# Optimization experiments

Measured on AMD Instinct MI355X. Metric: run time of the kernel, lower is better.

The kernel has to match this reference:

```python
import jax, jax.numpy as jnp
import numpy as np

TEMPERATURE = 1.0
CHUNK = 128  # node-block size for the curvature pass


def setup_inputs() -> dict:
    key = jax.random.key(0)
    k1, k2 = jax.random.split(key)
    N, D = 4096, 64
    x = jax.random.normal(k1, (N, D), dtype=jnp.float32)
    # sparse binary adjacency (avg degree ~16) + ring so min degree >= 2
    A = (jax.random.uniform(k2, (N, N)) < 0.004).astype(jnp.float32)
    i = jnp.arange(N)
    A = A.at[i, i].set(0.0)
    A = A.at[i, (i + 1) % N].set(1.0)
    A = A.at[(i + 1) % N, i].set(1.0)
    return {"node_embeddings": x, "adj_matrix": A}


def _physics_components(x, A):
    N, d = x.shape
    mask = A > 0
    deg = jnp.sum(A, axis=-1)                      # [N]

    # ---- total energy ----
    kinetic = jnp.sum(x * x, axis=-1)
    nb = A @ x                                     # neighbor aggregate [N,d]
    potential = -jnp.sum(x * nb, axis=-1)
    total_energy = kinetic + potential / (deg + 1e-8)

    # ---- local entropy over neighbor similarities ----
    xn = x / jnp.maximum(jnp.linalg.norm(x, axis=-1, keepdims=True), 1e-12)
    S = xn @ xn.T                                  # cosine sims [N,N]
    logits = jnp.where(mask, S / TEMPERATURE, -1e30)
    P = jax.nn.softmax(logits, axis=-1)            # masked softmax per row
    local_entropy = -jnp.sum(jnp.where(mask, P * jnp.log(P + 1e-8), 0.0), axis=-1)

    # ---- equilibrium deviation (5-NN local mean in embedding space) ----
    sq = jnp.sum(x * x, axis=-1)
    D2 = jnp.maximum(sq[:, None] + sq[None, :] - 2.0 * (x @ x.T), 1e-12)
    dist = jnp.sqrt(D2)                            # [N,N]
    _, idx = jax.lax.top_k(-dist, 6)               # smallest 6 (self first)
    local_means = jnp.mean(x[idx[:, 1:]], axis=1)  # [N,d]
    gdev = jnp.linalg.norm(x - jnp.mean(x, axis=0, keepdims=True), axis=-1)
    ldev = jnp.linalg.norm(x - local_means, axis=-1)
    equilibrium_deviation = 0.6 * gdev + 0.4 * ldev

    # ---- structural centrality ----
    en = jnp.linalg.norm(x, axis=-1)
    structural_centrality = 0.5 * deg / (N - 1) + 0.5 * en / jnp.max(en)

    # ---- information flow: unbiased var of neighbor sims ----
    ms = jnp.sum(jnp.where(mask, S, 0.0), axis=-1) / deg
    information_flow = jnp.sum(jnp.where(mask, (S - ms[:, None]) ** 2, 0.0), axis=-1) / (deg - 1.0)

    # ---- stability: 1/(1 + mean unbiased var of neighbor embeddings) ----
    m1 = nb / deg[:, None]
    ex2 = A @ (x * x)
    var_dim = (ex2 - deg[:, None] * m1 * m1) / (deg - 1.0)[:, None]
    stability = 1.0 / (1.0 + jnp.mean(var_dim, axis=-1))

    # ---- discrete curvature: 1 - mean pairwise cos angle of centered neighbors ----
    # mean_{j<k} u_j.u_k = (||sum u||^2 - sum ||u||^2) / (deg*(deg-1))
    def body(_, ids):
        xb = x[ids]                                 # [B,d]
        mb = mask[ids]                              # [B,N]
        c = x[None, :, :] - xb[:, None, :]          # [B,N,d]
        nrm = jnp.sqrt(jnp.maximum(jnp.sum(c * c, -1), 1e-12))
        u = jnp.where(mb[..., None], c / jnp.maximum(nrm, 1e-8)[..., None], 0.0)
        s = jnp.sum(u, axis=1)                      # [B,d]
        ssq = jnp.sum(u * u, axis=(1, 2))           # [B]
        db = jnp.sum(mb.astype(x.dtype), axis=-1)
        mean_cos = (jnp.sum(s * s, -1) - ssq) / (db * (db - 1.0))
        return None, 1.0 - mean_cos

    _, curv = jax.lax.scan(body, None, jnp.arange(N).reshape(-1, CHUNK))
    graph_curvature = curv.reshape(N)

    return (total_energy, local_entropy, equilibrium_deviation,
            structural_centrality, information_flow, stability, graph_curvature)


def reference(node_embeddings, adj_matrix):
    return _physics_components(node_embeddings, adj_matrix)
```

## Files before the change

### kernel.cpp

```cpp
#include <hip/hip_runtime.h>
#include <math.h>

#define NN 4096
#define DD 64
#define NSPLIT 16
#define JW 256

typedef _Float16 half8 __attribute__((ext_vector_type(8)));
typedef float f32x4 __attribute__((ext_vector_type(4)));

__device__ __forceinline__ unsigned sxu(unsigned v, int o){
  return (unsigned)__shfl_xor((int)v, o, 64);
}
__device__ __forceinline__ unsigned umn(unsigned a, unsigned b){ return a<b?a:b; }
__device__ __forceinline__ unsigned umx(unsigned a, unsigned b){ return a<b?b:a; }

__device__ __forceinline__ unsigned packkey32(float m, int j){
  float q = fmaf(m, 2048.f, 524288.f);
  q = fminf(fmaxf(q, 0.f), 1048575.f);
  return (((unsigned)q) << 12) | (unsigned)j;
}

__device__ __forceinline__ void ins5u(unsigned k, unsigned b[5]){
  bool c0=k<b[0], c1=k<b[1], c2=k<b[2], c3=k<b[3], c4=k<b[4];
  b[4] = c3 ? b[3] : (c4 ? k : b[4]);
  b[3] = c2 ? b[2] : (c3 ? k : b[3]);
  b[2] = c1 ? b[1] : (c2 ? k : b[2]);
  b[1] = c0 ? b[0] : (c1 ? k : b[1]);
  b[0] = c0 ? k : b[0];
}

__device__ __forceinline__ void mergeStage32(unsigned b[5], int st){
  unsigned p0=sxu(b[0],st),p1=sxu(b[1],st),p2=sxu(b[2],st),p3=sxu(b[3],st),p4=sxu(b[4],st);
  unsigned o0=umn(b[0],p0);
  unsigned o1=umn(umn(b[1],p1), umx(b[0],p0));
  unsigned o2=umn(umn(b[2],p2), umn(umx(b[0],p1),umx(b[1],p0)));
  unsigned o3=umn(umn(b[3],p3), umn(umx(b[0],p2), umn(umx(b[1],p1),umx(b[2],p0))));
  unsigned o4=umn(umn(b[4],p4), umn(umn(umx(b[0],p3),umx(b[1],p2)),
                                    umn(umx(b[2],p1),umx(b[3],p0))));
  b[0]=o0;b[1]=o1;b[2]=o2;b[3]=o3;b[4]=o4;
}

__device__ __forceinline__ void mergeLocal32(const unsigned a[5], const unsigned c[5], unsigned b[5]){
  b[0]=umn(a[0],c[0]);
  b[1]=umn(umn(a[1],c[1]), umx(a[0],c[0]));
  b[2]=umn(umn(a[2],c[2]), umn(umx(a[0],c[1]),umx(a[1],c[0])));
  b[3]=umn(umn(a[3],c[3]), umn(umx(a[0],c[2]), umn(umx(a[1],c[1]),umx(a[2],c[0]))));
  b[4]=umn(umn(a[4],c[4]), umn(umn(umx(a[0],c[3]),umx(a[1],c[2])),
                               umn(umx(a[2],c[1]),umx(a[3],c[0]))));
}

__global__ __launch_bounds__(256) void k_prec(const float* __restrict__ x,
                      float* __restrict__ sq,
                      _Float16* __restrict__ xh, _Float16* __restrict__ xl,
                      float* __restrict__ msum_part, float* __restrict__ maxsq_part){
  __shared__ float part[4][64];
  __shared__ float mxp[4];
  const int w = threadIdx.x>>6, lane = threadIdx.x&63;
  const int n0 = blockIdx.x*16 + w*4;
  float v0 = x[(size_t)(n0+0)*DD + lane];
  float v1 = x[(size_t)(n0+1)*DD + lane];
  float v2 = x[(size_t)(n0+2)*DD + lane];
  float v3 = x[(size_t)(n0+3)*DD + lane];
  float s0=v0*v0, s1=v1*v1, s2=v2*v2, s3=v3*v3;
#pragma unroll
  for(int o=1;o<64;o<<=1){
    s0 += __shfl_xor(s0,o,64); s1 += __shfl_xor(s1,o,64);
    s2 += __shfl_xor(s2,o,64); s3 += __shfl_xor(s3,o,64);
  }
  float vv[4] = {v0,v1,v2,v3};
  float ss[4] = {s0,s1,s2,s3};
#pragma unroll
  for(int q=0;q<4;q++){
    float v = vv[q];
    _Float16 h = (_Float16)v;
    _Float16 l = (_Float16)(v - (float)h);
    xh[(size_t)(n0+q)*DD+lane] = h;
    xl[(size_t)(n0+q)*DD+lane] = l;
    if(lane==0) sq[n0+q]=ss[q];
  }
  if(lane==0) mxp[w] = fmaxf(fmaxf(s0,s1), fmaxf(s2,s3));
  part[w][lane] = v0+v1+v2+v3; __syncthreads();
  if(w==0){
    msum_part[blockIdx.x*64 + lane] = part[0][lane]+part[1][lane]+part[2][lane]+part[3][lane];
    if(lane==0) maxsq_part[blockIdx.x] = fmaxf(fmaxf(mxp[0],mxp[1]), fmaxf(mxp[2],mxp[3]));
  }
}

__device__ __forceinline__ f32x4 gram6(const half8 J[4],
    half8 Ih0, half8 Ih1, half8 Il0, half8 Il1){
  const f32x4 z = {0.f,0.f,0.f,0.f};
  f32x4 a1 = __builtin_amdgcn_mfma_f32_16x16x32_f16(J[0], Ih0, z, 0,0,0);
  f32x4 a2 = __builtin_amdgcn_mfma_f32_16x16x32_f16(J[2], Ih0, z, 0,0,0);
  a1 = __builtin_amdgcn_mfma_f32_16x16x32_f16(J[1], Ih1, a1, 0,0,0);
  a2 = __builtin_amdgcn_mfma_f32_16x16x32_f16(J[3], Ih1, a2, 0,0,0);
  a1 = __builtin_amdgcn_mfma_f32_16x16x32_f16(J[0], Il0, a1, 0,0,0);
  a1 = __builtin_amdgcn_mfma_f32_16x16x32_f16(J[1], Il1, a1, 0,0,0);
  return a1 + a2;
}

__global__ __launch_bounds__(256, 4) void k_mega(
    const float* __restrict__ x, const float* __restrict__ A,
    const float* __restrict__ sq,
    const _Float16* __restrict__ xh, const _Float16* __restrict__ xl,
    unsigned* __restrict__ cand,
    const float* __restrict__ msum_part, const float* __restrict__ maxsq_part,
    float* __restrict__ msum, float* __restrict__ max_sq, float* __restrict__ deg_out,
    float* __restrict__ o_te, float* __restrict__ o_ent,
    float* __restrict__ o_if, float* __restrict__ o_st, float* __restrict__ o_cv)
{
  __shared__ int   nbr[4][128];
  __shared__ float Sval[4][128];
  __shared__ float rr[4][64];
  __shared__ float rm[4];
  __shared__ _Float16 jHi[2][512*8];
  __shared__ _Float16 jLo[2][512*8];
  const int bid = blockIdx.x;
  const int tid = threadIdx.x;
  const int w = tid>>6, lane = tid&63;

  if(bid == 0){
    float s = 0.f;
    for(int p=w; p<256; p+=4) s += msum_part[p*64 + lane];
    rr[w][lane] = s;
    float m = maxsq_part[w*64 + lane];
#pragma unroll
    for(int o=1;o<64;o<<=1) m = fmaxf(m, __shfl_xor(m,o,64));
    if(lane==0) rm[w] = m;
    __syncthreads();
    if(w==0){
      msum[lane] = rr[0][lane]+rr[1][lane]+rr[2][lane]+rr[3][lane];
      if(lane==0) max_sq[0] = fmaxf(fmaxf(rm[0],rm[1]), fmaxf(rm[2],rm[3]));
    }
    return;
  }

  const int t = bid - 1;
  if((t & 1) == 0){
    const int i = (t>>1)*4 + w;
    const float xid = x[(size_t)i*DD + lane];
    const float sqi = sq[i];
    const float eni = sqrtf(sqi);
    const float4* A4 = (const float4*)(A + (size_t)i*NN);

    int deg = 0;
    for(int ch=0; ch<4; ++ch){
      float4 av[4];
#pragma unroll
      for(int qq=0; qq<4; ++qq) av[qq] = A4[lane + 64*(ch*4+qq)];
      int c = 0;
#pragma unroll
      for(int qq=0; qq<4; ++qq)
        c += (av[qq].x>0.f)+(av[qq].y>0.f)+(av[qq].z>0.f)+(av[qq].w>0.f);
      int sc = c;
#pragma unroll
      for(int o=1;o<64;o<<=1){ int v=__shfl_up(sc,o,64); if(lane>=o) sc+=v; }
      int off = deg + sc - c;
#pragma unroll
      for(int qq=0; qq<4; ++qq){
        int jb = 4*(lane + 64*(ch*4+qq));
        if(av[qq].x>0.f){ if(off<128) nbr[w][off]=jb+0; off++; }
        if(av[qq].y>0.f){ if(off<128) nbr[w][off]=jb+1; off++; }
        if(av[qq].z>0.f){ if(off<128) nbr[w][off]=jb+2; off++; }
        if(av[qq].w>0.f){ if(off<128) nbr[w][off]=jb+3; off++; }
      }
      deg += __shfl(sc, 63, 64);
    }

    const float degf = (float)deg;
    const int dmax = min(deg, 128);
    float nb_d=0.f, ex2_d=0.f, s_d=0.f, ssq=0.f;

    for(int c0=0; c0<dmax; c0+=8){
      int jq[8]; float aq[8], qq[8];
#pragma unroll
      for(int q=0;q<8;q++) jq[q] = nbr[w][min(c0+q, dmax-1)];
#pragma unroll
      for(int q=0;q<8;q++) aq[q] = x[(size_t)jq[q]*DD + lane];
#pragma unroll
      for(int q=0;q<8;q++) qq[q] = sq[jq[q]];
      asm volatile("" :: "v"(aq[0]), "v"(aq[1]), "v"(aq[2]), "v"(aq[3]),
                         "v"(aq[4]), "v"(aq[5]), "v"(aq[6]), "v"(aq[7]));
      float p[8];
#pragma unroll
      for(int q=0;q<8;q++) p[q] = xid*aq[q];
#pragma unroll
      for(int o=1;o<64;o<<=1){
#pragma unroll
        for(int q=0;q<8;q++) p[q] += __shfl_xor(p[q],o,64);
      }
#pragma unroll
      for(int q=0;q<8;q++){
        const bool valid = (c0+q) < deg;
        float c2 = fmaxf(sqi + qq[q] - 2.0f*p[q], 1e-12f);
        float inv = 1.0f/fmaxf(sqrtf(c2), 1e-8f);
        nb_d  += valid ? aq[q] : 0.f;
        ex2_d += valid ? aq[q]*aq[q] : 0.f;
        s_d   += valid ? (aq[q]-xid)*inv : 0.f;
        ssq   += valid ? c2*inv*inv : 0.f;
        if(valid && lane==q) Sval[w][c0+q] = p[q]/(eni*sqrtf(qq[q]));
      }
    }

    float t0 = xid*nb_d;
    float m1 = nb_d/degf;
    float t1 = (ex2_d - degf*m1*m1)/(degf-1.0f);
    float t2 = s_d*s_d;
    float t3 = 0.f, t4 = 0.f;
    for(int s=lane; s<dmax; s+=64){ float v=Sval[w][s]; t3 += expf(v); t4 += v; }
#pragma unroll
    for(int o=1;o<64;o<<=1){
      t0 += __shfl_xor(t0,o,64); t1 += __shfl_xor(t1,o,64); t2 += __shfl_xor(t2,o,64);
      t3 += __shfl_xor(t3,o,64); t4 += __shfl_xor(t4,o,64);
    }
    const float pot = t0, varm = t1*(1.0f/DD), s2 = t2, se = t3, ms = t4/degf;

    float e0=0.f, e1=0.f;
    const float inv_se = 1.0f/se;
    for(int s=lane; s<dmax; s+=64){
      float v = Sval[w][s];
      float pp = expf(v)*inv_se;
      e0 -= pp*logf(pp + 1e-8f);
      float dv = v-ms; e1 += dv*dv;
    }
#pragma unroll
    for(int o=1;o<64;o<<=1){ e0 += __shfl_xor(e0,o,64); e1 += __shfl_xor(e1,o,64); }

    if(lane==0){
      o_te[i]  = sqi - pot/(degf + 1e-8f);
      o_ent[i] = e0;
      o_if[i]  = e1/(degf-1.0f);
      o_st[i]  = 1.0f/(1.0f + varm);
      o_cv[i]  = 1.0f - (s2 - ssq)/(degf*(degf-1.0f));
      deg_out[i] = degf;
    }
  } else {
    const int kid = t >> 1;
    const int split = kid & (NSPLIT-1);
    const int strip = (kid >> 4)*4 + w;
    const int ibase = strip*16, j0 = split*JW;
    const int col = lane & 15, kg = lane >> 4;
    const int vo = col*DD + kg*8;
    const int myi = ibase + col;

#define STAGE(BUF, CH) { \
    _Pragma("unroll") \
    for(int q_=0;q_<2;q_++){ \
      int g_ = q_*256 + tid; \
      int r_ = g_ >> 3; \
      int c_ = (g_ & 7) ^ (r_ & 7); \
      const _Float16* sH_ = xh + (size_t)(j0 + (CH)*64 + r_)*DD + c_*8; \
      const _Float16* sL_ = xl + (size_t)(j0 + (CH)*64 + r_)*DD + c_*8; \
      __builtin_amdgcn_global_load_lds( \
        (const __attribute__((address_space(1))) unsigned int*)sH_, \
        (__attribute__((address_space(3))) unsigned int*)(jHi[BUF] + g_*8), 16, 0, 0); \
      __builtin_amdgcn_global_load_lds( \
        (const __attribute__((address_space(1))) unsigned int*)sL_, \
        (__attribute__((address_space(3))) unsigned int*)(jLo[BUF] + g_*8), 16, 0, 0); \
    } }

    STAGE(0, 0);

    const _Float16* pih = xh + (size_t)ibase*DD + vo;
    const _Float16* pil = xl + (size_t)ibase*DD + vo;
    const half8 Ih0 = *(const half8*)(pih);
    const half8 Ih1 = *(const half8*)(pih+32);
    const half8 Il0 = *(const half8*)(pil);
    const half8 Il1 = *(const half8*)(pil+32);

    unsigned bA[5], bB[5];
#pragma unroll
    for(int k=0;k<5;k++){ bA[k]=0xFFFFFFFFu; bB[k]=0xFFFFFFFFu; }

#pragma unroll
    for(int ch=0; ch<4; ch++){
      __syncthreads();
      if(ch<3) STAGE((ch+1)&1, ch+1);
      const _Float16* bh = jHi[ch&1];
      const _Float16* bl = jLo[ch&1];
      const int jb0 = j0 + ch*64 + kg*4;
      float4 sq0 = *(const float4*)(sq + jb0);
      float4 sq1 = *(const float4*)(sq + jb0 + 16);
      float4 sq2 = *(const float4*)(sq + jb0 + 32);
      float4 sq3 = *(const float4*)(sq + jb0 + 48);

      half8 JT[4];
#define TILE(TT, SQV, LIST) { \
      const int rl_ = (TT)*16 + col; \
      const int sw_ = rl_ & 7; \
      JT[0] = *(const half8*)(bh + (rl_*8 + ( kg      ^ sw_))*8); \
      JT[1] = *(const half8*)(bh + (rl_*8 + ((kg + 4) ^ sw_))*8); \
      JT[2] = *(const half8*)(bl + (rl_*8 + ( kg      ^ sw_))*8); \
      JT[3] = *(const half8*)(bl + (rl_*8 + ((kg + 4) ^ sw_))*8); \
      f32x4 d_ = gram6(JT, Ih0, Ih1, Il0, Il1); \
      float sv_[4] = {SQV.x, SQV.y, SQV.z, SQV.w}; \
      const int jt0_ = jb0 + (TT)*16; \
      _Pragma("unroll") \
      for(int r_=0;r_<4;r_++){ \
        unsigned kk_ = packkey32(fmaf(-2.0f, d_[r_], sv_[r_]), jt0_+r_); \
        kk_ = (jt0_+r_==myi) ? 0xFFFFFFFFu : kk_; \
        ins5u(kk_, LIST); \
      } }

      TILE(0, sq0, bA);
      TILE(1, sq1, bB);
      TILE(2, sq2, bA);
      TILE(3, sq3, bB);
#undef TILE
    }
#undef STAGE

    unsigned b[5];
    mergeLocal32(bA, bB, b);
    mergeStage32(b, 16);
    mergeStage32(b, 32);

    if(kg==0){
#pragma unroll
      for(int k=0;k<5;k++)
        cand[((size_t)myi*NSPLIT + split)*5 + k] = b[k];
    }
  }
}

__global__ __launch_bounds__(256) void k_nnsel(
    const float* __restrict__ x, const unsigned* __restrict__ cand,
    const float* __restrict__ msum, const float* __restrict__ max_sq,
    const float* __restrict__ deg, const float* __restrict__ sq,
    float* __restrict__ o_eq, float* __restrict__ o_sc)
{
  const int w = threadIdx.x>>6, l = threadIdx.x&63;
  const int i = blockIdx.x*4 + w;
  const unsigned* cr = cand + (size_t)i*(NSPLIT*5);
  unsigned c0 = cr[l];
  unsigned c1 = (l < 16) ? cr[64+l] : 0xFFFFFFFFu;

  int sel[5];
#pragma unroll
  for(int k=0;k<5;k++){
    unsigned d = umn(c0,c1);
#pragma unroll
    for(int o=1;o<64;o<<=1) d = umn(d, sxu(d,o));
    sel[k] = (int)(d & 0xFFFu);
    if(c0==d) c0=0xFFFFFFFFu;
    else if(c1==d) c1=0xFFFFFFFFu;
  }

  float smv=0.f;
#pragma unroll
  for(int k=0;k<5;k++) smv += x[(size_t)sel[k]*DD + l];
  float xiv = x[(size_t)i*DD + l];
  float lv = xiv - smv*0.2f;
  float gv = xiv - msum[l]*(1.0f/NN);
  float pl = lv*lv, pg = gv*gv;
#pragma unroll
  for(int o=1;o<64;o<<=1){ pl += __shfl_xor(pl,o,64); pg += __shfl_xor(pg,o,64); }
  if(l==0){
    o_eq[i] = 0.6f*sqrtf(pg) + 0.4f*sqrtf(pl);
    o_sc[i] = 0.5f*deg[i]/(float)(NN-1) + 0.5f*sqrtf(sq[i])/sqrtf(max_sq[0]);
  }
}

extern "C" void kernel_launch(void* const* d_in, const int* in_sizes, int n_in,
                              void* d_out, int out_size, void* d_ws, size_t ws_size,
                              hipStream_t stream) {
  const float* x = (const float*)d_in[0];
  const float* A = (const float*)d_in[1];
  float* out = (float*)d_out;
  float* ws  = (float*)d_ws;
  float*     sq        = ws;
  float*     msum      = ws + 4096;
  float*     max_sq    = ws + 4160;
  float*     deg       = ws + 4224;
  float*     msum_part = ws + 8320;
  float*     maxsq_part= ws + 24704;
  _Float16*  xh        = (_Float16*)(ws + 24960);
  _Float16*  xl        = (_Float16*)(ws + 156032);
  unsigned*  cand      = (unsigned*)(ws + 287104);

  k_prec<<<NN/16, 256, 0, stream>>>(x, sq, xh, xl, msum_part, maxsq_part);
  k_mega<<<NN/2 + 1, 256, 0, stream>>>(x, A, sq, xh, xl, cand,
                                       msum_part, maxsq_part, msum, max_sq, deg,
                                       out, out+NN, out+4*NN, out+5*NN, out+6*NN);
  k_nnsel<<<NN/4, 256, 0, stream>>>(x, cand, msum, max_sq, deg, sq,
                                    out+2*NN, out+3*NN);
}
```

Baseline: 56.97 us.

## Single-buffer KNN tile staging and use ballot-based neighbor compaction

The k-NN gram branch drops the double-buffered LDS staging for a single buffer. Each chunk is now loaded and then fenced with syncthreads before compute and again after it. This halves LDS use, which may raise occupancy, but loses the overlap of global loads with MFMA work. Separately, the neighbor-list compaction in the row branch replaces the shuffle prefix scan with a per-element ballot and popcount, trading the log-step scan for 16 ballots per chunk.

```diff
diff --git a/kernel.cpp b/kernel.cpp
--- a/kernel.cpp
+++ b/kernel.cpp
@@ -113,8 +113,8 @@
   __shared__ float Sval[4][128];
   __shared__ float rr[4][64];
   __shared__ float rm[4];
-  __shared__ _Float16 jHi[2][512*8];
-  __shared__ _Float16 jLo[2][512*8];
+  __shared__ _Float16 jHi[512*8];
+  __shared__ _Float16 jLo[512*8];
   const int bid = blockIdx.x;
   const int tid = threadIdx.x;
   const int w = tid>>6, lane = tid&63;
@@ -142,30 +142,31 @@
     const float sqi = sq[i];
     const float eni = sqrtf(sqi);
     const float4* A4 = (const float4*)(A + (size_t)i*NN);
-
-    int deg = 0;
+    const unsigned long long below = (1ull << lane) - 1ull;
+
+    int base = 0;
+#define COMPACT(VAL, JJ) { \
+    bool p_ = (VAL) > 0.f; \
+    unsigned long long m_ = __ballot(p_); \
+    int ofs_ = base + (int)__popcll(m_ & below); \
+    if(p_ && ofs_ < 128) nbr[w][ofs_] = (JJ); \
+    base += (int)__popcll(m_); \
+  }
     for(int ch=0; ch<4; ++ch){
       float4 av[4];
 #pragma unroll
       for(int qq=0; qq<4; ++qq) av[qq] = A4[lane + 64*(ch*4+qq)];
-      int c = 0;
-#pragma unroll
-      for(int qq=0; qq<4; ++qq)
-        c += (av[qq].x>0.f)+(av[qq].y>0.f)+(av[qq].z>0.f)+(av[qq].w>0.f);
-      int sc = c;
-#pragma unroll
-      for(int o=1;o<64;o<<=1){ int v=__shfl_up(sc,o,64); if(lane>=o) sc+=v; }
-      int off = deg + sc - c;
 #pragma unroll
       for(int qq=0; qq<4; ++qq){
         int jb = 4*(lane + 64*(ch*4+qq));
-        if(av[qq].x>0.f){ if(off<128) nbr[w][off]=jb+0; off++; }
-        if(av[qq].y>0.f){ if(off<128) nbr[w][off]=jb+1; off++; }
-        if(av[qq].z>0.f){ if(off<128) nbr[w][off]=jb+2; off++; }
-        if(av[qq].w>0.f){ if(off<128) nbr[w][off]=jb+3; off++; }
+        COMPACT(av[qq].x, jb+0);
+        COMPACT(av[qq].y, jb+1);
+        COMPACT(av[qq].z, jb+2);
+        COMPACT(av[qq].w, jb+3);
       }
-      deg += __shfl(sc, 63, 64);
-    }
+    }
+#undef COMPACT
+    const int deg = base;
 
     const float degf = (float)deg;
     const int dmax = min(deg, 128);
@@ -243,7 +244,7 @@
     const int vo = col*DD + kg*8;
     const int myi = ibase + col;
 
-#define STAGE(BUF, CH) { \
+#define STAGE(CH) { \
     _Pragma("unroll") \
     for(int q_=0;q_<2;q_++){ \
       int g_ = q_*256 + tid; \
@@ -253,13 +254,11 @@
       const _Float16* sL_ = xl + (size_t)(j0 + (CH)*64 + r_)*DD + c_*8; \
       __builtin_amdgcn_global_load_lds( \
         (const __attribute__((address_space(1))) unsigned int*)sH_, \
-        (__attribute__((address_space(3))) unsigned int*)(jHi[BUF] + g_*8), 16, 0, 0); \
+        (__attribute__((address_space(3))) unsigned int*)(jHi + g_*8), 16, 0, 0); \
       __builtin_amdgcn_global_load_lds( \
         (const __attribute__((address_space(1))) unsigned int*)sL_, \
-        (__attribute__((address_space(3))) unsigned int*)(jLo[BUF] + g_*8), 16, 0, 0); \
+        (__attribute__((address_space(3))) unsigned int*)(jLo + g_*8), 16, 0, 0); \
     } }
-
-    STAGE(0, 0);
 
     const _Float16* pih = xh + (size_t)ibase*DD + vo;
     const _Float16* pil = xl + (size_t)ibase*DD + vo;
@@ -274,24 +273,22 @@
 
 #pragma unroll
     for(int ch=0; ch<4; ch++){
-      __syncthreads();
-      if(ch<3) STAGE((ch+1)&1, ch+1);
-      const _Float16* bh = jHi[ch&1];
-      const _Float16* bl = jLo[ch&1];
+      STAGE(ch);
       const int jb0 = j0 + ch*64 + kg*4;
       float4 sq0 = *(const float4*)(sq + jb0);
       float4 sq1 = *(const float4*)(sq + jb0 + 16);
       float4 sq2 = *(const float4*)(sq + jb0 + 32);
       float4 sq3 = *(const float4*)(sq + jb0 + 48);
+      __syncthreads();
 
       half8 JT[4];
 #define TILE(TT, SQV, LIST) { \
       const int rl_ = (TT)*16 + col; \
       const int sw_ = rl_ & 7; \
-      JT[0] = *(const half8*)(bh + (rl_*8 + ( kg      ^ sw_))*8); \
-      JT[1] = *(const half8*)(bh + (rl_*8 + ((kg + 4) ^ sw_))*8); \
-      JT[2] = *(const half8*)(bl + (rl_*8 + ( kg      ^ sw_))*8); \
-      JT[3] = *(const half8*)(bl + (rl_*8 + ((kg + 4) ^ sw_))*8); \
+      JT[0] = *(const half8*)(jHi + (rl_*8 + ( kg      ^ sw_))*8); \
+      JT[1] = *(const half8*)(jHi + (rl_*8 + ((kg + 4) ^ sw_))*8); \
+      JT[2] = *(const half8*)(jLo + (rl_*8 + ( kg      ^ sw_))*8); \
+      JT[3] = *(const half8*)(jLo + (rl_*8 + ((kg + 4) ^ sw_))*8); \
       f32x4 d_ = gram6(JT, Ih0, Ih1, Il0, Il1); \
       float sv_[4] = {SQV.x, SQV.y, SQV.z, SQV.w}; \
       const int jt0_ = jb0 + (TT)*16; \
@@ -307,6 +304,7 @@
       TILE(2, sq2, bA);
       TILE(3, sq3, bB);
 #undef TILE
+      __syncthreads();
     }
 #undef STAGE
 
```

Measured after the change: 56.79 us. No clear change (-0.3%).
